# Performance work log

Measured on AMD Instinct MI355X. Metric: run time of the kernel, lower is better.

Reference implementation:

```python
import jax, jax.numpy as jnp
import numpy as np


def setup_inputs() -> dict:
    key = jax.random.key(0)
    ks = jax.random.split(key, 5)
    B, H, S, D = 4, 16, 2048, 64
    queries = jax.random.normal(ks[0], (B, H, S, D), dtype=jnp.float32)
    keys = jax.random.normal(ks[1], (B, H, S, D), dtype=jnp.float32)
    values = jax.random.normal(ks[2], (B, H, S, D), dtype=jnp.float32)
    W_out = jax.random.normal(ks[3], (D, D), dtype=jnp.float32) / np.sqrt(D)
    b_out = jax.random.normal(ks[4], (D,), dtype=jnp.float32) * 0.01
    return {"queries": queries, "keys": keys, "values": values, "W_out": W_out, "b_out": b_out}


def reference(queries, keys, values, W_out, b_out):
    # scores: [B,H,S,S] = Q K^T / sqrt(D)
    scale = 1.0 / np.sqrt(queries.shape[-1]).astype(np.float32)
    scores = jnp.einsum("bhqd,bhkd->bhqk", queries, keys) * scale
    # concrete attention distribution: softmax over keys axis
    distr = jax.nn.softmax(scores, axis=-1)
    # weighted sum of values: [B,H,S,D]
    out = jnp.einsum("bhqk,bhkd->bhqd", distr, values)
    # out projection (nn.Linear: x @ W^T + b)
    out = jnp.einsum("bhqd,ed->bhqe", out, W_out) + b_out
    return out
```

## Files before the change

### kernel.cpp

```cpp
#include <hip/hip_runtime.h>
#include <math.h>


typedef __attribute__((ext_vector_type(8)))  short    s16x8;
typedef __attribute__((ext_vector_type(4)))  float    f32x4;
typedef __attribute__((ext_vector_type(16))) float    f32x16;
typedef __attribute__((ext_vector_type(4)))  unsigned u32x4;

#define KQSCALE 0.18033688011112042f

__device__ __forceinline__ unsigned short f2bu(float x) {
    __bf16 v = (__bf16)x;
    return __builtin_bit_cast(unsigned short, v);
}
__device__ __forceinline__ short f2b(float x) { return (short)f2bu(x); }
__device__ __forceinline__ float b2f(short s) {
    __bf16 v = __builtin_bit_cast(__bf16, (unsigned short)s);
    return (float)v;
}
__device__ __forceinline__ unsigned pack2(float lo, float hi) {
    return (unsigned)f2bu(lo) | ((unsigned)f2bu(hi) << 16);
}
__device__ __forceinline__ int swzK(int row) { return (row & 7) << 4; }
__device__ __forceinline__ int swzV(int row) { return (((row >> 4) & 3) ^ (row & 7)) << 4; }

#define PLSWAP(x, y) asm("v_permlane32_swap_b32 %0, %1" : "+v"(x), "+v"(y))

#define BARRIER()                                              \
    do {                                                       \
        asm volatile("s_waitcnt lgkmcnt(0)" ::: "memory");     \
        __builtin_amdgcn_s_barrier();                          \
    } while (0)

#define QK2(SA, SB, KsC, KT)                                                    \
    f32x16 SA = {}; f32x16 SB = {};                                             \
    __builtin_amdgcn_s_setprio(1);                                              \
    _Pragma("unroll")                                                           \
    for (int dt = 0; dt < 4; ++dt) {                                            \
        const int krow = (KT) * 32 + q32;                                       \
        s16x8 kf = *(s16x8*)((KsC) + krow * 128 +                               \
                             ((dt * 32 + h * 16) ^ swzK(krow)));                \
        SA = __builtin_amdgcn_mfma_f32_32x32x16_bf16(kf, qfA[dt], SA, 0, 0, 0); \
        SB = __builtin_amdgcn_mfma_f32_32x32x16_bf16(kf, qfB[dt], SB, 0, 0, 0); \
    }                                                                           \
    __builtin_amdgcn_s_setprio(0);

#define PVQ2(SA, SB, VtC, KT, T)                                               \
    do {                                                                       \
        const float ea0 = __builtin_amdgcn_exp2f((SA)[8 * (T) + 0]);           \
        const float ea1 = __builtin_amdgcn_exp2f((SA)[8 * (T) + 1]);           \
        const float ea2 = __builtin_amdgcn_exp2f((SA)[8 * (T) + 2]);           \
        const float ea3 = __builtin_amdgcn_exp2f((SA)[8 * (T) + 3]);           \
        const float ea4 = __builtin_amdgcn_exp2f((SA)[8 * (T) + 4]);           \
        const float ea5 = __builtin_amdgcn_exp2f((SA)[8 * (T) + 5]);           \
        const float ea6 = __builtin_amdgcn_exp2f((SA)[8 * (T) + 6]);           \
        const float ea7 = __builtin_amdgcn_exp2f((SA)[8 * (T) + 7]);           \
        const float eb0 = __builtin_amdgcn_exp2f((SB)[8 * (T) + 0]);           \
        const float eb1 = __builtin_amdgcn_exp2f((SB)[8 * (T) + 1]);           \
        const float eb2 = __builtin_amdgcn_exp2f((SB)[8 * (T) + 2]);           \
        const float eb3 = __builtin_amdgcn_exp2f((SB)[8 * (T) + 3]);           \
        const float eb4 = __builtin_amdgcn_exp2f((SB)[8 * (T) + 4]);           \
        const float eb5 = __builtin_amdgcn_exp2f((SB)[8 * (T) + 5]);           \
        const float eb6 = __builtin_amdgcn_exp2f((SB)[8 * (T) + 6]);           \
        const float eb7 = __builtin_amdgcn_exp2f((SB)[8 * (T) + 7]);           \
        unsigned ka0 = pack2(ea0, ea1), ka1 = pack2(ea2, ea3);                 \
        unsigned ka2 = pack2(ea4, ea5), ka3 = pack2(ea6, ea7);                 \
        PLSWAP(ka0, ka2);                                                      \
        PLSWAP(ka1, ka3);                                                      \
        u32x4 pwA; pwA[0] = ka0; pwA[1] = ka1; pwA[2] = ka2; pwA[3] = ka3;     \
        const s16x8 pA_ = __builtin_bit_cast(s16x8, pwA);                      \
        unsigned kb0 = pack2(eb0, eb1), kb1 = pack2(eb2, eb3);                 \
        unsigned kb2 = pack2(eb4, eb5), kb3 = pack2(eb6, eb7);                 \
        PLSWAP(kb0, kb2);                                                      \
        PLSWAP(kb1, kb3);                                                      \
        u32x4 pwB; pwB[0] = kb0; pwB[1] = kb1; pwB[2] = kb2; pwB[3] = kb3;     \
        const s16x8 pB_ = __builtin_bit_cast(s16x8, pwB);                      \
        const int kbo = (KT) * 64 + (T) * 32 + h * 16;                         \
        __builtin_amdgcn_s_setprio(1);                                         \
        s16x8 vf0 = *(s16x8*)((VtC) + q32 * 128 + (kbo ^ swzV(q32)));          \
        s16x8 vf1 = *(s16x8*)((VtC) + (32 + q32) * 128 + (kbo ^ swzV(32 + q32))); \
        accA0 = __builtin_amdgcn_mfma_f32_32x32x16_bf16(pA_, vf0, accA0, 0, 0, 0); \
        accB0 = __builtin_amdgcn_mfma_f32_32x32x16_bf16(pB_, vf0, accB0, 0, 0, 0); \
        accA1 = __builtin_amdgcn_mfma_f32_32x32x16_bf16(pA_, vf1, accA1, 0, 0, 0); \
        accB1 = __builtin_amdgcn_mfma_f32_32x32x16_bf16(pB_, vf1, accB1, 0, 0, 0); \
        rsA = __builtin_amdgcn_mfma_f32_32x32x16_bf16(pA_, onesV, rsA, 0, 0, 0); \
        rsB = __builtin_amdgcn_mfma_f32_32x32x16_bf16(pB_, onesV, rsB, 0, 0, 0); \
        __builtin_amdgcn_s_setprio(0);                                         \
    } while (0)

__global__ __launch_bounds__(256, 2) void attn_fused(
    const float* __restrict__ Qg, const float* __restrict__ Kg,
    const float* __restrict__ Vg, const float* __restrict__ Wg,
    const float* __restrict__ bg, float* __restrict__ outg)
{
    __shared__ __align__(16) char smem[32768];
    char* Ks0 = smem;
    char* Vt0 = smem + 8192;
    char* Ks1 = smem + 16384;
    char* Vt1 = smem + 24576;

    const int tid  = threadIdx.x;
    const int wave = tid >> 6;
    const int lane = tid & 63;
    const int h    = lane >> 5;
    const int q32  = lane & 31;
    const int g    = lane >> 4;
    const int c    = lane & 15;

    const int orig = blockIdx.x;
    const int wg   = (orig & 7) * 64 + (orig >> 3);
    const int bh   = wg >> 3;
    const int qblk = wg & 7;

    const float* Qh = Qg + (size_t)bh * (2048 * 64);
    const float* Kh = Kg + (size_t)bh * (2048 * 64);
    const float* Vh = Vg + (size_t)bh * (2048 * 64);
    float*       Oh = outg + (size_t)bh * (2048 * 64);

    const int qbaseA = qblk * 256 + wave * 32;
    const int qbaseB = qbaseA + 128;

    const int srow = tid >> 2;
    const int scb  = (tid & 3) * 16;
    const int vk   = (tid >> 3) * 2;
    const int vd8  = (tid & 7) * 8;
    const int kOff = srow * 64 + scb;
    const int vOff = vk * 64 + vd8;

    f32x4 qLa[4], qLb[4], qLc[4], qLd[4];
#pragma unroll
    for (int dt = 0; dt < 4; ++dt) {
        const float* sA = Qh + (size_t)(qbaseA + q32) * 64 + dt * 16 + h * 8;
        const float* sB = Qh + (size_t)(qbaseB + q32) * 64 + dt * 16 + h * 8;
        qLa[dt] = *(const f32x4*)(sA);
        qLb[dt] = *(const f32x4*)(sA + 4);
        qLc[dt] = *(const f32x4*)(sB);
        qLd[dt] = *(const f32x4*)(sB + 4);
    }

    f32x4 rT0, rT1, rT2, rT3;

    auto issueK = [&](int chunk) {
        const float* p = Kh + (size_t)chunk * 4096 + kOff;
        rT0 = *(const f32x4*)(p);
        rT1 = *(const f32x4*)(p + 4);
        rT2 = *(const f32x4*)(p + 8);
        rT3 = *(const f32x4*)(p + 12);
    };
    auto issueV = [&](int chunk) {
        const float* p = Vh + (size_t)chunk * 4096 + vOff;
        rT0 = *(const f32x4*)(p);
        rT1 = *(const f32x4*)(p + 4);
        rT2 = *(const f32x4*)(p + 64);
        rT3 = *(const f32x4*)(p + 68);
    };
    auto stageK = [&](char* KsD) {
        u32x4 wA, wB;
        wA[0] = pack2(rT0[0], rT0[1]); wA[1] = pack2(rT0[2], rT0[3]);
        wA[2] = pack2(rT1[0], rT1[1]); wA[3] = pack2(rT1[2], rT1[3]);
        wB[0] = pack2(rT2[0], rT2[1]); wB[1] = pack2(rT2[2], rT2[3]);
        wB[2] = pack2(rT3[0], rT3[1]); wB[3] = pack2(rT3[2], rT3[3]);
        const int base = srow * 128;
        const int sw   = swzK(srow);
        *(u32x4*)(KsD + base + ((scb * 2) ^ sw))      = wA;
        *(u32x4*)(KsD + base + ((scb * 2 + 16) ^ sw)) = wB;
    };
    auto stageV = [&](char* VtD) {
#pragma unroll
        for (int i = 0; i < 8; ++i) {
            const int d = vd8 + i;
            const float lo = (i < 4) ? rT0[i & 3] : rT1[i & 3];
            const float hi = (i < 4) ? rT2[i & 3] : rT3[i & 3];
            *(unsigned*)(VtD + d * 128 + ((2 * vk) ^ swzV(d))) = pack2(lo, hi);
        }
    };

    s16x8 qfA[4], qfB[4];
#pragma unroll
    for (int dt = 0; dt < 4; ++dt) {
        u32x4 fA, fB;
        fA[0] = pack2(qLa[dt][0] * KQSCALE, qLa[dt][1] * KQSCALE);
        fA[1] = pack2(qLa[dt][2] * KQSCALE, qLa[dt][3] * KQSCALE);
        fA[2] = pack2(qLb[dt][0] * KQSCALE, qLb[dt][1] * KQSCALE);
        fA[3] = pack2(qLb[dt][2] * KQSCALE, qLb[dt][3] * KQSCALE);
        fB[0] = pack2(qLc[dt][0] * KQSCALE, qLc[dt][1] * KQSCALE);
        fB[1] = pack2(qLc[dt][2] * KQSCALE, qLc[dt][3] * KQSCALE);
        fB[2] = pack2(qLd[dt][0] * KQSCALE, qLd[dt][1] * KQSCALE);
        fB[3] = pack2(qLd[dt][2] * KQSCALE, qLd[dt][3] * KQSCALE);
        qfA[dt] = __builtin_bit_cast(s16x8, fA);
        qfB[dt] = __builtin_bit_cast(s16x8, fB);
    }

    f32x16 accA0 = {}, accA1 = {}, accB0 = {}, accB1 = {};
    f32x16 rsA = {}, rsB = {};
    u32x4 onesW;
    onesW[0] = 0x3F803F80u; onesW[1] = 0x3F803F80u;
    onesW[2] = 0x3F803F80u; onesW[3] = 0x3F803F80u;
    const s16x8 onesV = __builtin_bit_cast(s16x8, onesW);

    auto one_iter = [&](char* KsC, char* VtC, char* KsN, char* VtN, int kc) {
        QK2(s0A, s0B, KsC, 0);
        PVQ2(s0A, s0B, VtC, 0, 0);
        if (kc < 31) {
            stageK(KsN);
            __builtin_amdgcn_sched_barrier(0);
            issueV(kc + 1);
        }
        PVQ2(s0A, s0B, VtC, 0, 1);
        QK2(s1A, s1B, KsC, 1);
        PVQ2(s1A, s1B, VtC, 1, 0);
        if (kc < 31) {
            stageV(VtN);
            __builtin_amdgcn_sched_barrier(0);
            if (kc < 30) issueK(kc + 2);
        }
        PVQ2(s1A, s1B, VtC, 1, 1);
        BARRIER();
    };

    issueK(0);
    stageK(Ks0);
    __builtin_amdgcn_sched_barrier(0);
    issueV(0);
    stageV(Vt0);
    __builtin_amdgcn_sched_barrier(0);
    issueK(1);
    BARRIER();

    for (int kc = 0; kc < 32; kc += 2) {
        one_iter(Ks0, Vt0, Ks1, Vt1, kc);
        one_iter(Ks1, Vt1, Ks0, Vt0, kc + 1);
    }

#pragma unroll
    for (int r = 0; r < 16; ++r) {
        const float ivA = __builtin_amdgcn_rcpf(rsA[r]);
        const float ivB = __builtin_amdgcn_rcpf(rsB[r]);
        accA0[r] *= ivA;  accA1[r] *= ivA;
        accB0[r] *= ivB;  accB1[r] *= ivB;
    }

    auto stageO = [&](const f32x16& a0, const f32x16& a1) {
        char* Ow = smem + wave * 8192;
#pragma unroll
        for (int r = 0; r < 16; ++r) {
            const int row = (r & 3) + 8 * (r >> 2) + 4 * h;
            const int sw  = (row & 7) << 5;
            *(float*)(Ow + row * 256 + ((q32 * 4)       ^ sw)) = a0[r];
            *(float*)(Ow + row * 256 + ((128 + q32 * 4) ^ sw)) = a1[r];
        }
    };
    auto project = [&](int qb) {
        char* Ow = smem + wave * 8192;
        f32x4 po[2][4];
#pragma unroll
        for (int rt = 0; rt < 2; ++rt)
#pragma unroll
            for (int et = 0; et < 4; ++et) {
                po[rt][et][0] = 0.f; po[rt][et][1] = 0.f;
                po[rt][et][2] = 0.f; po[rt][et][3] = 0.f;
            }
#pragma unroll
        for (int kh = 0; kh < 2; ++kh) {
            s16x8 ahi[2], alo[2];
#pragma unroll
            for (int rt = 0; rt < 2; ++rt) {
                const int row = rt * 16 + c;
                const int rb  = row * 256;
                const int rsw = (row & 7) << 5;
                const int o0  = (kh * 128 + g * 32) ^ rsw;
                f32x4 x0 = *(f32x4*)(Ow + rb + o0);
                f32x4 x1 = *(f32x4*)(Ow + rb + o0 + 16);
                s16x8 hh8, lo8;
#pragma unroll
                for (int j = 0; j < 4; ++j) {
                    const short hv = f2b(x0[j]);
                    hh8[j] = hv;  lo8[j] = f2b(x0[j] - b2f(hv));
                }
#pragma unroll
                for (int j = 0; j < 4; ++j) {
                    const short hv = f2b(x1[j]);
                    hh8[4 + j] = hv;  lo8[4 + j] = f2b(x1[j] - b2f(hv));
                }
                ahi[rt] = hh8; alo[rt] = lo8;
            }
#pragma unroll
            for (int et = 0; et < 4; ++et) {
                const float* ws = Wg + (et * 16 + c) * 64 + kh * 32 + g * 8;
                f32x4 w0 = *(const f32x4*)ws;
                f32x4 w1 = *(const f32x4*)(ws + 4);
                s16x8 whi, wlo;
#pragma unroll
                for (int j = 0; j < 4; ++j) {
                    const short hv = f2b(w0[j]);
                    whi[j] = hv;  wlo[j] = f2b(w0[j] - b2f(hv));
                }
#pragma unroll
                for (int j = 0; j < 4; ++j) {
                    const short hv = f2b(w1[j]);
                    whi[4 + j] = hv;  wlo[4 + j] = f2b(w1[j] - b2f(hv));
                }
#pragma unroll
                for (int rt = 0; rt < 2; ++rt) {
                    po[rt][et] = __builtin_amdgcn_mfma_f32_16x16x32_bf16(ahi[rt], whi, po[rt][et], 0, 0, 0);
                    po[rt][et] = __builtin_amdgcn_mfma_f32_16x16x32_bf16(alo[rt], whi, po[rt][et], 0, 0, 0);
                    po[rt][et] = __builtin_amdgcn_mfma_f32_16x16x32_bf16(ahi[rt], wlo, po[rt][et], 0, 0, 0);
                }
            }
        }
#pragma unroll
        for (int et = 0; et < 4; ++et) {
            const float bb = bg[et * 16 + c];
#pragma unroll
            for (int rt = 0; rt < 2; ++rt)
#pragma unroll
                for (int r = 0; r < 4; ++r) {
                    const int qrow = qb + rt * 16 + 4 * g + r;
                    Oh[(size_t)qrow * 64 + et * 16 + c] = po[rt][et][r] + bb;
                }
        }
    };

    BARRIER();
    stageO(accA0, accA1);
    BARRIER();
    project(qbaseA);
    BARRIER();
    stageO(accB0, accB1);
    BARRIER();
    project(qbaseB);
}

extern "C" void kernel_launch(void* const* d_in, const int* in_sizes, int n_in,
                              void* d_out, int out_size, void* d_ws, size_t ws_size,
                              hipStream_t stream) {
    const float* Q = (const float*)d_in[0];
    const float* K = (const float*)d_in[1];
    const float* V = (const float*)d_in[2];
    const float* W = (const float*)d_in[3];
    const float* b = (const float*)d_in[4];
    float* out = (float*)d_out;
    hipLaunchKernelGGL(attn_fused, dim3(512), dim3(256), 0, stream, Q, K, V, W, b, out);
}
```

Baseline: 98.96 us.

## Use separate K and V prefetch registers to prefetch V a full chunk ahead

Splits the shared staging registers into dedicated K and V register sets, so the V loads for chunk kc+1 are issued a whole iteration earlier alongside the K loads instead of mid-iteration. The sched_barriers that serialized staging and issuing are removed. This lengthens the latency-hiding window for global V loads, at the cost of 16 more live VGPRs, which could lower occupancy or cause spills.

```diff
diff --git a/kernel.cpp b/kernel.cpp
--- a/kernel.cpp
+++ b/kernel.cpp
@@ -138,28 +138,29 @@
         qLd[dt] = *(const f32x4*)(sB + 4);
     }
 
-    f32x4 rT0, rT1, rT2, rT3;
+    f32x4 rK0, rK1, rK2, rK3;
+    f32x4 rV0, rV1, rV2, rV3;
 
     auto issueK = [&](int chunk) {
         const float* p = Kh + (size_t)chunk * 4096 + kOff;
-        rT0 = *(const f32x4*)(p);
-        rT1 = *(const f32x4*)(p + 4);
-        rT2 = *(const f32x4*)(p + 8);
-        rT3 = *(const f32x4*)(p + 12);
+        rK0 = *(const f32x4*)(p);
+        rK1 = *(const f32x4*)(p + 4);
+        rK2 = *(const f32x4*)(p + 8);
+        rK3 = *(const f32x4*)(p + 12);
     };
     auto issueV = [&](int chunk) {
         const float* p = Vh + (size_t)chunk * 4096 + vOff;
-        rT0 = *(const f32x4*)(p);
-        rT1 = *(const f32x4*)(p + 4);
-        rT2 = *(const f32x4*)(p + 64);
-        rT3 = *(const f32x4*)(p + 68);
+        rV0 = *(const f32x4*)(p);
+        rV1 = *(const f32x4*)(p + 4);
+        rV2 = *(const f32x4*)(p + 64);
+        rV3 = *(const f32x4*)(p + 68);
     };
     auto stageK = [&](char* KsD) {
         u32x4 wA, wB;
-        wA[0] = pack2(rT0[0], rT0[1]); wA[1] = pack2(rT0[2], rT0[3]);
-        wA[2] = pack2(rT1[0], rT1[1]); wA[3] = pack2(rT1[2], rT1[3]);
-        wB[0] = pack2(rT2[0], rT2[1]); wB[1] = pack2(rT2[2], rT2[3]);
-        wB[2] = pack2(rT3[0], rT3[1]); wB[3] = pack2(rT3[2], rT3[3]);
+        wA[0] = pack2(rK0[0], rK0[1]); wA[1] = pack2(rK0[2], rK0[3]);
+        wA[2] = pack2(rK1[0], rK1[1]); wA[3] = pack2(rK1[2], rK1[3]);
+        wB[0] = pack2(rK2[0], rK2[1]); wB[1] = pack2(rK2[2], rK2[3]);
+        wB[2] = pack2(rK3[0], rK3[1]); wB[3] = pack2(rK3[2], rK3[3]);
         const int base = srow * 128;
         const int sw   = swzK(srow);
         *(u32x4*)(KsD + base + ((scb * 2) ^ sw))      = wA;
@@ -169,8 +170,8 @@
 #pragma unroll
         for (int i = 0; i < 8; ++i) {
             const int d = vd8 + i;
-            const float lo = (i < 4) ? rT0[i & 3] : rT1[i & 3];
-            const float hi = (i < 4) ? rT2[i & 3] : rT3[i & 3];
+            const float lo = (i < 4) ? rV0[i & 3] : rV1[i & 3];
+            const float hi = (i < 4) ? rV2[i & 3] : rV3[i & 3];
             *(unsigned*)(VtD + d * 128 + ((2 * vk) ^ swzV(d))) = pack2(lo, hi);
         }
     };
@@ -203,28 +204,25 @@
         PVQ2(s0A, s0B, VtC, 0, 0);
         if (kc < 31) {
             stageK(KsN);
-            __builtin_amdgcn_sched_barrier(0);
-            issueV(kc + 1);
+            if (kc < 30) issueK(kc + 2);
         }
         PVQ2(s0A, s0B, VtC, 0, 1);
         QK2(s1A, s1B, KsC, 1);
         PVQ2(s1A, s1B, VtC, 1, 0);
         if (kc < 31) {
             stageV(VtN);
-            __builtin_amdgcn_sched_barrier(0);
-            if (kc < 30) issueK(kc + 2);
+            if (kc < 30) issueV(kc + 2);
         }
         PVQ2(s1A, s1B, VtC, 1, 1);
         BARRIER();
     };
 
     issueK(0);
+    issueV(0);
     stageK(Ks0);
-    __builtin_amdgcn_sched_barrier(0);
-    issueV(0);
     stageV(Vt0);
-    __builtin_amdgcn_sched_barrier(0);
     issueK(1);
+    issueV(1);
     BARRIER();
 
     for (int kc = 0; kc < 32; kc += 2) {
```

Result: no change. 99.96 us (+1.0%).
